# Kernel optimization log

Hardware: AMD Instinct MI355X
Metric: run time of the kernel (lower is better)

Reference implementation:

```python
import jax, jax.numpy as jnp
import numpy as np

T = 2048        # flat document tokens
D = 400         # word_emb (doc emb dim)
H2 = 400        # 2 * lstm_hidden_size
MAXW = 10       # max_ment_width
C = T * MAXW    # candidate spans
M = 600         # pruned mentions
A = 100         # max_ment_dist antecedents
FS = 20         # feature_size
HID = 150       # scorer hidden size
NG = 7          # num genres
BIN_WIDTHS = [1, 1, 1, 1, 1, 3, 8, 16, 32, 1]  # sums to 65, covers clamp(dist, max=64)
MENT_IN = 4 * 200 + FS + D          # 1220
ANTE_IN = 3 * MENT_IN + 3 * FS      # 3720


def setup_inputs() -> dict:
    key = jax.random.key(0)
    ks = jax.random.split(key, 24)
    w = lambda k, shp: (jax.random.normal(k, shp, dtype=jnp.float32) * 0.02)
    flat_doc_embs = jax.random.normal(ks[0], (T, D), dtype=jnp.float32)
    flat_lstm_out = jax.random.normal(ks[1], (T, H2), dtype=jnp.float32)
    # all spans up to width MAXW starting at each token (as produced upstream)
    cand_starts = jnp.repeat(jnp.arange(T), MAXW)
    cand_ends = jnp.minimum(cand_starts + jnp.tile(jnp.arange(MAXW), T), T - 1)
    top_ment_idx = jnp.sort(jax.random.choice(ks[2], C, (M,), replace=False))
    speaker_ids = jax.random.randint(ks[3], (T,), 0, 4)
    # antecedent index matrix exactly as built in get_antecedents
    i = jnp.arange(M)[:, None]
    j = jnp.arange(A)[None, :]
    antecedents = jnp.where(j < i, j, 0) + jnp.maximum(i - A, 0)
    antecedents_len = jnp.minimum(jnp.arange(M), A)
    bins = jnp.asarray(np.repeat(np.arange(len(BIN_WIDTHS)), BIN_WIDTHS), dtype=jnp.int32)
    return {
        'flat_doc_embs': flat_doc_embs, 'flat_lstm_out': flat_lstm_out,
        'cand_starts': cand_starts, 'cand_ends': cand_ends,
        'top_ment_idx': top_ment_idx, 'antecedents': antecedents,
        'antecedents_len': antecedents_len, 'speaker_ids': speaker_ids,
        'genre_id': 3, 'bins': bins,
        'width_table': w(ks[4], (MAXW, FS)), 'speaker_table': w(ks[5], (2, FS)),
        'genre_table': w(ks[6], (NG, FS)), 'dist_table': w(ks[7], (len(BIN_WIDTHS), FS)),
        'W_span': w(ks[8], (H2, 1)), 'b_span': jnp.zeros((1,), jnp.float32),
        'ms_w1': w(ks[9], (MENT_IN, HID)), 'ms_b1': jnp.zeros((HID,), jnp.float32),
        'ms_w2': w(ks[10], (HID, HID)), 'ms_b2': jnp.zeros((HID,), jnp.float32),
        'ms_w3': w(ks[11], (HID, 1)), 'ms_b3': jnp.zeros((1,), jnp.float32),
        'as_w1': w(ks[12], (ANTE_IN, HID)), 'as_b1': jnp.zeros((HID,), jnp.float32),
        'as_w2': w(ks[13], (HID, HID)), 'as_b2': jnp.zeros((HID,), jnp.float32),
        'as_w3': w(ks[14], (HID, 1)), 'as_b3': jnp.zeros((1,), jnp.float32),
    }


def _scorer(x, w1, b1, w2, b2, w3, b3):
    h = jax.nn.relu(x @ w1 + b1)
    h = jax.nn.relu(h @ w2 + b2)
    return (h @ w3 + b3)[..., 0]


def _ment_embedding(flat_doc_embs, flat_lstm_out, starts, ends, width_table, W_span, b_span):
    start_embs = flat_lstm_out[starts]            # [N, H2]
    end_embs = flat_lstm_out[ends]                # [N, H2]
    width = ends - starts + 1                     # [N]
    width_embs = width_table[width - 1]           # [N, FS]
    doc_len = flat_doc_embs.shape[0]
    span_idxs = jnp.minimum(jnp.arange(MAXW)[None, :] + starts[:, None], doc_len - 1)  # [N, W]
    ment_doc_embs = flat_doc_embs[span_idxs]      # [N, W, D]
    head_logits = (flat_lstm_out @ W_span + b_span)[:, 0]   # [T]
    logits = head_logits[span_idxs]               # [N, W]
    mask = jnp.arange(MAXW)[None, :] < width[:, None]
    logits = logits + jnp.log(mask.astype(jnp.float32))
    attn = jax.nn.softmax(logits, axis=1)[:, :, None]        # [N, W, 1]
    head_embs = (attn * ment_doc_embs).sum(axis=1)           # [N, D]
    return jnp.concatenate((start_embs, end_embs, width_embs, head_embs), axis=1)


def reference(flat_doc_embs, flat_lstm_out, cand_starts, cand_ends, top_ment_idx,
              antecedents, antecedents_len, speaker_ids, genre_id, bins,
              width_table, speaker_table, genre_table, dist_table, W_span, b_span,
              ms_w1, ms_b1, ms_w2, ms_b2, ms_w3, ms_b3,
              as_w1, as_b1, as_w2, as_b2, as_w3, as_b3):
    cand_embs = _ment_embedding(flat_doc_embs, flat_lstm_out, cand_starts, cand_ends,
                                width_table, W_span, b_span)          # [C, 1220]
    cand_scores = _scorer(cand_embs, ms_w1, ms_b1, ms_w2, ms_b2, ms_w3, ms_b3)  # [C]
    ment_starts = cand_starts[top_ment_idx]
    ment_embs = cand_embs[top_ment_idx]                                # [M, 1220]
    ment_scores = cand_scores[top_ment_idx]                            # [M]
    ment_speakers = speaker_ids[ment_starts]                           # [M]
    # antecedent_embedding
    num_ment, max_ante = antecedents.shape
    genre_emb = jnp.broadcast_to(genre_table[genre_id][None, None, :], (num_ment, max_ante, FS))
    ante_speakers = ment_speakers[antecedents]                         # [M, A]
    same_speaker = (ment_speakers[:, None] == ante_speakers).astype(jnp.int32)
    speaker_emb = speaker_table[same_speaker]                          # [M, A, FS]
    ante_dist = jnp.arange(num_ment)[:, None] - antecedents
    ante_dist_emb = dist_table[bins[jnp.minimum(ante_dist, 64)]]       # [M, A, FS]
    feature_emb = jnp.concatenate((speaker_emb, genre_emb, ante_dist_emb), axis=2)
    antecedent_emb = ment_embs[antecedents]                            # [M, A, 1220]
    ment_rep = jnp.broadcast_to(ment_embs[:, None, :], antecedent_emb.shape)
    similarity_emb = antecedent_emb * ment_rep
    ante_full = jnp.concatenate((ment_rep, antecedent_emb, similarity_emb, feature_emb), axis=2)
    ante_scores = _scorer(ante_full, as_w1, as_b1, as_w2, as_b2, as_w3, as_b3)   # [M, A]
    ante_mask = jnp.arange(max_ante)[None, :] < antecedents_len[:, None]
    ante_scores = ante_scores + jnp.log(ante_mask.astype(jnp.float32))
    coref = ante_scores + ment_scores[:, None] + ment_scores[antecedents]
    coref_score = jnp.concatenate((jnp.zeros((num_ment, 1), jnp.float32), coref), axis=1)
    return coref_score
```

## Files before the change

### kernel.cpp

```cpp
#include <hip/hip_runtime.h>
#include <math.h>

typedef __attribute__((ext_vector_type(8))) short short8v;
typedef __attribute__((ext_vector_type(4))) float float4v;
typedef unsigned int u32;
typedef unsigned short u16;

#define T_     2048
#define D_     400
#define H2_    400
#define MAXW_  10
#define M_     600
#define A_     100
#define FS_    20
#define HID_   150
#define HP_    160
#define MIN_   1220
#define KP_    1280
#define NCOL_  101
#define L2K_   192

#define NEGBIG_ (-1.0e30f)

#define OB_MSC   8192u
#define OB_PM    10752u
#define OB_PA    394752u
#define OB_SPKC  778752u
#define OB_GB    780032u
#define OB_DC    780672u
#define OB_MSPK  787072u
#define OB_H1W   789632u
#define OB_MEBF  1173632u
#define OB_WSIM  2709632u
#define OB_WK2   3119232u
#define OB_W2A   4348032u
#define OB_END   4409472u

__device__ __forceinline__ float bflo(u32 u){ u32 v = u << 16; return __builtin_bit_cast(float, v); }
__device__ __forceinline__ float bfhi(u32 u){ u32 v = u & 0xFFFF0000u; return __builtin_bit_cast(float, v); }
__device__ __forceinline__ u16 f2bf(float f){
  u32 u = __builtin_bit_cast(u32, f);
  u32 r = (u + 0x7FFFu + ((u >> 16) & 1u)) >> 16;
  return (u16)r;
}
__device__ __forceinline__ u32 cvtpk(float lo, float hi){
  u32 r; asm("v_cvt_pk_bf16_f32 %0, %1, %2" : "=v"(r) : "v"(lo), "v"(hi)); return r;
}

__global__ __launch_bounds__(256) void kb_prep(
    const float* __restrict__ msw1, const float* __restrict__ asw1,
    const float* __restrict__ asw2, const float* __restrict__ asb1,
    const float* __restrict__ spkt, const float* __restrict__ gent,
    const float* __restrict__ distt, const int* __restrict__ gid,
    u16* __restrict__ wsim, u16* __restrict__ wk2, u16* __restrict__ w2a,
    float* __restrict__ spk_c, float* __restrict__ gb, float* __restrict__ dc) {
  int z = blockIdx.z;
  if (z == 5) {
    if (blockIdx.x | blockIdx.y) return;
    int h = threadIdx.x;
    if (h >= HP_) return;
    if (h >= HID_) {
      spk_c[h] = 0.f; spk_c[HP_ + h] = 0.f; gb[h] = 0.f;
      for (int d = 0; d < 10; d++) dc[d * HP_ + h] = 0.f;
      return;
    }
    float s0 = 0.f, s1 = 0.f, g = asb1[h];
    int gi = gid[0];
    for (int f = 0; f < FS_; f++) {
      float w = asw1[(3660 + f) * HID_ + h];
      s0 += spkt[f] * w;
      s1 += spkt[FS_ + f] * w;
      g += gent[gi * FS_ + f] * asw1[(3680 + f) * HID_ + h];
    }
    spk_c[h] = s0; spk_c[HP_ + h] = s1; gb[h] = g;
    for (int d = 0; d < 10; d++) {
      float acc = 0.f;
      for (int f = 0; f < FS_; f++) acc += distt[d * FS_ + f] * asw1[(3700 + f) * HID_ + h];
      dc[d * HP_ + h] = acc;
    }
    return;
  }
  const float* src; u16* dst; int S, Rpad, R;
  if (z == 0)      { src = asw1 + 2440 * HID_; dst = wsim;            S = KP_;  Rpad = KP_;  R = MIN_; }
  else if (z == 1) { src = msw1;               dst = wk2;             S = KP_;  Rpad = KP_;  R = MIN_; }
  else if (z == 2) { src = asw1;               dst = wk2 + 160 * KP_; S = KP_;  Rpad = KP_;  R = MIN_; }
  else if (z == 3) { src = asw1 + 1220 * HID_; dst = wk2 + 320 * KP_; S = KP_;  Rpad = KP_;  R = MIN_; }
  else             { src = asw2;               dst = w2a;             S = L2K_; Rpad = L2K_; R = HID_;
                     if (blockIdx.x >= 6) return; }
  __shared__ float tile[32][33];
  int tx = threadIdx.x & 31, ty = threadIdx.x >> 5;
  int rb = blockIdx.x * 32, cb = blockIdx.y * 32;
#pragma unroll
  for (int it = 0; it < 4; it++) {
    int r = rb + ty + it * 8, c = cb + tx;
    tile[ty + it * 8][tx] = (r < R && c < HID_) ? src[(size_t)r * HID_ + c] : 0.f;
  }
  __syncthreads();
#pragma unroll
  for (int it = 0; it < 4; it++) {
    int c = cb + ty + it * 8, r = rb + tx;
    if (c < HP_ && r < Rpad) dst[(size_t)c * S + r] = f2bf(tile[tx][ty + it * 8]);
  }
}

__global__ __launch_bounds__(256) void ka_ment_emb(
    const float* __restrict__ doc, const float* __restrict__ lstm,
    const int* __restrict__ cs, const int* __restrict__ ce,
    const int* __restrict__ tmi, const int* __restrict__ spk,
    const float* __restrict__ wtab, const float* __restrict__ Wsp,
    const float* __restrict__ bsp,
    u16* __restrict__ mebf, int* __restrict__ mspk) {
  __shared__ float sl[MAXW_];
  int b = blockIdx.x, tid = threadIdx.x;
  int idx = tmi[b];
  int s = cs[idx], e = ce[idx];
  int width = e - s + 1;
  int wv = tid >> 6, lane = tid & 63;
  for (int w = wv; w < width; w += 4) {
    float acc = 0.f;
    for (int k = lane; k < H2_; k += 64) acc += lstm[(s + w) * H2_ + k] * Wsp[k];
    for (int off = 32; off; off >>= 1) acc += __shfl_down(acc, off);
    if (lane == 0) sl[w] = acc + bsp[0];
  }
  u16* row = mebf + (size_t)b * KP_;
  for (int d = tid; d < D_; d += 256) {
    row[d]      = f2bf(lstm[s * H2_ + d]);
    row[D_ + d] = f2bf(lstm[e * H2_ + d]);
  }
  if (tid < FS_) row[2 * D_ + tid] = f2bf(wtab[(width - 1) * FS_ + tid]);
  for (int d = tid; d < (KP_ - MIN_); d += 256) row[MIN_ + d] = 0;
  __syncthreads();
  float wl[MAXW_];
  float mx = -1e30f;
  for (int w = 0; w < width; w++) { wl[w] = sl[w]; mx = fmaxf(mx, wl[w]); }
  float sum = 0.f;
  for (int w = 0; w < width; w++) { wl[w] = expf(wl[w] - mx); sum += wl[w]; }
  float inv = 1.f / sum;
  for (int d = tid; d < D_; d += 256) {
    float acc = 0.f;
    for (int w = 0; w < width; w++) acc += wl[w] * doc[(s + w) * D_ + d];
    row[2 * D_ + FS_ + d] = f2bf(acc * inv);
  }
  if (tid == 0) mspk[b] = spk[s];
}

__global__ __launch_bounds__(256) void k2_mfma(
    const u16* __restrict__ mebf, const u16* __restrict__ wk2,
    const float* __restrict__ msb1,
    float* __restrict__ h1w, float* __restrict__ Pm, float* __restrict__ Pa) {
  __shared__ __align__(16) char lds[20480];
  int mt = blockIdx.x, ct = blockIdx.y;
  int tid = threadIdx.x, w = tid >> 6, l = tid & 63, l15 = l & 15, oct = l >> 4;
  int m0 = mt * 128;
  const u16* Bb = wk2 + (size_t)ct * 160 * KP_;
  u32 aswz = (u32)(l15 & 7) << 4;
  float4v acc[2][10];
#pragma unroll
  for (int p = 0; p < 2; p++)
#pragma unroll
    for (int h = 0; h < 10; h++) acc[p][h] = (float4v)0.f;
  int arow[2];
#pragma unroll
  for (int p = 0; p < 2; p++) {
    int r = m0 + (2 * w + p) * 16 + l15;
    arow[p] = (r < M_) ? r : (M_ - 1);
  }
  for (int kt = 0; kt < 20; kt++) {
    int k0 = kt * 64;
#pragma unroll
    for (int it = 0; it < 5; it++) {
      int ee = tid + it * 256;
      int r = ee >> 3, sg = ee & 7;
      uint4 v = *(const uint4*)(Bb + (size_t)r * KP_ + k0 + sg * 8);
      *(uint4*)(lds + (u32)(r * 128) + (((u32)(sg * 16)) ^ ((u32)(r & 7) << 4))) = v;
    }
    short8v A[2][2];
#pragma unroll
    for (int p = 0; p < 2; p++)
#pragma unroll
      for (int ks2 = 0; ks2 < 2; ks2++)
        A[p][ks2] = *(const short8v*)(mebf + (size_t)arow[p] * KP_ + k0 + ks2 * 32 + oct * 8);
    __syncthreads();
#pragma unroll
    for (int ks2 = 0; ks2 < 2; ks2++) {
      u32 inner = ((u32)(ks2 * 64 + oct * 16)) ^ aswz;
#pragma unroll
      for (int hf = 0; hf < 10; hf++) {
        short8v B = *(const short8v*)(lds + (u32)((hf * 16 + l15) * 128) + inner);
        acc[0][hf] = __builtin_amdgcn_mfma_f32_16x16x32_bf16(A[0][ks2], B, acc[0][hf], 0, 0, 0);
        acc[1][hf] = __builtin_amdgcn_mfma_f32_16x16x32_bf16(A[1][ks2], B, acc[1][hf], 0, 0, 0);
      }
    }
    __syncthreads();
  }
#pragma unroll
  for (int p = 0; p < 2; p++) {
    int mb = m0 + (2 * w + p) * 16 + oct * 4;
#pragma unroll
    for (int hf = 0; hf < 10; hf++) {
      int c = hf * 16 + l15;
#pragma unroll
      for (int r = 0; r < 4; r++) {
        int m = mb + r;
        if (m < M_) {
          float v = acc[p][hf][r];
          if (ct == 0) {
            float bias = (c < HID_) ? msb1[c] : 0.f;
            h1w[m * HP_ + c] = fmaxf(v + bias, 0.f);
          } else if (ct == 1) {
            Pm[m * HP_ + c] = v;
          } else {
            Pa[m * HP_ + c] = v;
          }
        }
      }
    }
  }
}

__global__ __launch_bounds__(256) void k5_msc(
    const float* __restrict__ h1w, const float* __restrict__ w2, const float* __restrict__ b2,
    const float* __restrict__ w3, const float* __restrict__ b3, float* __restrict__ msc) {
  __shared__ float h1s[HID_];
  __shared__ float h2s[HID_];
  __shared__ float red[4];
  int i = blockIdx.x, tid = threadIdx.x;
  if (tid < HID_) h1s[tid] = h1w[i * HP_ + tid];
  __syncthreads();
  if (tid < HID_) {
    float a = b2[tid];
    for (int k = 0; k < HID_; k++) a += h1s[k] * w2[k * HID_ + tid];
    h2s[tid] = fmaxf(a, 0.f);
  }
  __syncthreads();
  float p = (tid < HID_) ? h2s[tid] * w3[tid] : 0.f;
  for (int off = 32; off; off >>= 1) p += __shfl_down(p, off, 64);
  if ((tid & 63) == 0) red[tid >> 6] = p;
  __syncthreads();
  if (tid == 0) msc[i] = red[0] + red[1] + red[2] + red[3] + b3[0];
}

__global__ __launch_bounds__(256) void k4_pairs(
    const u16* __restrict__ mebf, const u16* __restrict__ wsim, const u16* __restrict__ w2a,
    const float* __restrict__ Pm, const float* __restrict__ Pa,
    const float* __restrict__ spkc, const float* __restrict__ gb, const float* __restrict__ dc,
    const int* __restrict__ mspk, const int* __restrict__ bins,
    const float* __restrict__ msc,
    const float* __restrict__ ab2, const float* __restrict__ aw3, const float* __restrict__ ab3,
    float* __restrict__ out) {
  __shared__ __align__(16) char lds[49152];
  int bid = blockIdx.x;
  int i = (bid & 7) * 75 + (bid >> 3);
  int tid = threadIdx.x, w = tid >> 6, l = tid & 63, l15 = l & 15, oct = l >> 4;
  int len = min(i, A_);
  int jbase = max(i - A_, 0);
  if (len == 0) {
    if (tid == 0) out[0] = 0.f;
    if (tid < A_) out[1 + tid] = NEGBIG_;
    return;
  }
  {
    const uint4* src = (const uint4*)(mebf + (size_t)i * KP_);
    uint4* dst = (uint4*)(lds + 36864);
    if (tid < 160) dst[tid] = src[tid];
  }
  __syncthreads();

  float4v acc[2][10];
#pragma unroll
  for (int p = 0; p < 2; p++)
#pragma unroll
    for (int h = 0; h < 10; h++) acc[p][h] = (float4v)0.f;

  int arow = tid >> 1;
  int khe = (tid & 1) * 32;
  int jrow = min(jbase + arow, M_ - 1);
  const u16* ejrow = mebf + (size_t)jrow * KP_;
  u32 pwr_base = 20480u + (u32)arow * 128u;
  u32 pwr_swz  = (u32)(arow & 7) << 4;
  u32 kh2 = (u32)khe * 2u;
  int r0 = 2 * w * 16 + l15, r1 = r0 + 16;
  u32 aswz = (u32)(l15 & 7) << 4;

  uint4 pe[4];
#pragma unroll
  for (int q = 0; q < 4; q++) pe[q] = *(const uint4*)(ejrow + khe + q * 8);

  for (int kt = 0; kt < 20; kt++) {
    int k0 = kt * 64;
#pragma unroll
    for (int it = 0; it < 5; it++) {
      int ee = tid + it * 256;
      int r = ee >> 3, sg = ee & 7;
      uint4 v = *(const uint4*)(wsim + (size_t)r * KP_ + k0 + sg * 8);
      *(uint4*)(lds + (u32)(r * 128) + (((u32)(sg * 16)) ^ ((u32)(r & 7) << 4))) = v;
    }
    const uint4* eis = (const uint4*)((const u16*)(lds + 36864) + k0 + khe);
#pragma unroll
    for (int q = 0; q < 4; q++) {
      uint4 ej = pe[q];
      uint4 ei = eis[q];
      const u32* pj = (const u32*)&ej;
      const u32* pi = (const u32*)&ei;
      u32 o[4];
#pragma unroll
      for (int c = 0; c < 4; c++) {
        float a0 = bflo(pj[c]) * bflo(pi[c]);
        float a1 = bfhi(pj[c]) * bfhi(pi[c]);
        o[c] = cvtpk(a0, a1);
      }
      uint4 ov = make_uint4(o[0], o[1], o[2], o[3]);
      *(uint4*)(lds + (pwr_base + ((kh2 + (u32)q * 16u) ^ pwr_swz))) = ov;
    }
    {
      int kn = (kt < 19) ? (kt + 1) * 64 : kt * 64;
#pragma unroll
      for (int q = 0; q < 4; q++) pe[q] = *(const uint4*)(ejrow + kn + khe + q * 8);
    }
    __syncthreads();
#pragma unroll
    for (int ks2 = 0; ks2 < 2; ks2++) {
      u32 inner = ((u32)(ks2 * 64 + oct * 16)) ^ aswz;
      short8v A0 = *(const short8v*)(lds + 20480u + (u32)r0 * 128u + inner);
      short8v A1 = *(const short8v*)(lds + 20480u + (u32)r1 * 128u + inner);
#pragma unroll
      for (int hf = 0; hf < 10; hf++) {
        short8v B = *(const short8v*)(lds + (u32)((hf * 16 + l15) * 128) + inner);
        acc[0][hf] = __builtin_amdgcn_mfma_f32_16x16x32_bf16(A0, B, acc[0][hf], 0, 0, 0);
        acc[1][hf] = __builtin_amdgcn_mfma_f32_16x16x32_bf16(A1, B, acc[1][hf], 0, 0, 0);
      }
    }
    __syncthreads();
  }

  for (int x = tid; x < 2048; x += 256) {
    int a = x >> 4, q = x & 15;
    u32 byte = 32768u + (u32)a * 128u + (((u32)(64 + q * 4)) ^ ((u32)(a & 7) << 4));
    *(u32*)(lds + byte) = 0u;
  }
  int mi = mspk[i];
#pragma unroll
  for (int hf = 0; hf < 10; hf++) {
    int h = hf * 16 + l15;
    float pmh = Pm[i * HP_ + h];
    float gbh = gb[h];
    int t = h >> 6, kkb = (h & 63) * 2;
#pragma unroll
    for (int p = 0; p < 2; p++) {
      int ab = (2 * w + p) * 16 + oct * 4;
#pragma unroll
      for (int r = 0; r < 4; r++) {
        int a = ab + r;
        int ju = jbase + a;
        int jr = min(ju, M_ - 1);
        int same = (mspk[jr] == mi) ? 1 : 0;
        int dist = min(max(i - ju, 0), 64);
        int bin = bins[dist];
        float v = acc[p][hf][r] + pmh + gbh + Pa[jr * HP_ + h]
                + spkc[same * HP_ + h] + dc[bin * HP_ + h];
        v = fmaxf(v, 0.f);
        u32 byte = (u32)t * 16384u + (u32)a * 128u + (((u32)kkb) ^ ((u32)(a & 7) << 4));
        *(u16*)(lds + byte) = f2bf(v);
      }
    }
  }
  __syncthreads();

  float4v b2acc[2][10];
#pragma unroll
  for (int p = 0; p < 2; p++)
#pragma unroll
    for (int h = 0; h < 10; h++) b2acc[p][h] = (float4v)0.f;
#pragma unroll
  for (int t = 0; t < 3; t++) {
#pragma unroll
    for (int ks2 = 0; ks2 < 2; ks2++) {
      u32 inner = ((u32)(ks2 * 64 + oct * 16)) ^ aswz;
      u32 tb = (u32)t * 16384u;
      short8v A0 = *(const short8v*)(lds + tb + (u32)r0 * 128u + inner);
      short8v A1 = *(const short8v*)(lds + tb + (u32)r1 * 128u + inner);
      int ke = t * 64 + ks2 * 32 + oct * 8;
#pragma unroll
      for (int hf = 0; hf < 10; hf++) {
        short8v B = *(const short8v*)(w2a + (size_t)(hf * 16 + l15) * L2K_ + ke);
        b2acc[0][hf] = __builtin_amdgcn_mfma_f32_16x16x32_bf16(A0, B, b2acc[0][hf], 0, 0, 0);
        b2acc[1][hf] = __builtin_amdgcn_mfma_f32_16x16x32_bf16(A1, B, b2acc[1][hf], 0, 0, 0);
      }
    }
  }

  float part[2][4] = {{0.f,0.f,0.f,0.f},{0.f,0.f,0.f,0.f}};
#pragma unroll
  for (int hf = 0; hf < 10; hf++) {
    int h = hf * 16 + l15;
    float bias = (h < HID_) ? ab2[h] : 0.f;
    float w3v  = (h < HID_) ? aw3[h] : 0.f;
#pragma unroll
    for (int p = 0; p < 2; p++)
#pragma unroll
      for (int r = 0; r < 4; r++) {
        float hv = fmaxf(b2acc[p][hf][r] + bias, 0.f);
        part[p][r] += hv * w3v;
      }
  }
#pragma unroll
  for (int m = 1; m <= 8; m <<= 1) {
#pragma unroll
    for (int p = 0; p < 2; p++)
#pragma unroll
      for (int r = 0; r < 4; r++) part[p][r] += __shfl_xor(part[p][r], m, 64);
  }
  float b3 = ab3[0];
  float msci = msc[i];
  if (l15 == 0) {
#pragma unroll
    for (int p = 0; p < 2; p++)
#pragma unroll
      for (int r = 0; r < 4; r++) {
        int a = (2 * w + p) * 16 + oct * 4 + r;
        if (a < A_) {
          float res = (a < len) ? (part[p][r] + b3 + msci + msc[jbase + a]) : NEGBIG_;
          out[(size_t)i * NCOL_ + 1 + a] = res;
        }
      }
  }
  if (tid == 0) out[(size_t)i * NCOL_] = 0.f;
}

extern "C" void kernel_launch(void* const* d_in, const int* in_sizes, int n_in,
                              void* d_out, int out_size, void* d_ws, size_t ws_size,
                              hipStream_t stream) {
  const float* doc   = (const float*)d_in[0];
  const float* lstm  = (const float*)d_in[1];
  const int*   cs    = (const int*)d_in[2];
  const int*   ce    = (const int*)d_in[3];
  const int*   tmi   = (const int*)d_in[4];
  const int*   spk   = (const int*)d_in[7];
  const int*   gid   = (const int*)d_in[8];
  const int*   bins  = (const int*)d_in[9];
  const float* wtab  = (const float*)d_in[10];
  const float* spkt  = (const float*)d_in[11];
  const float* gent  = (const float*)d_in[12];
  const float* distt = (const float*)d_in[13];
  const float* Wsp   = (const float*)d_in[14];
  const float* bsp   = (const float*)d_in[15];
  const float* msw1  = (const float*)d_in[16];
  const float* msb1  = (const float*)d_in[17];
  const float* msw2  = (const float*)d_in[18];
  const float* msb2  = (const float*)d_in[19];
  const float* msw3  = (const float*)d_in[20];
  const float* msb3  = (const float*)d_in[21];
  const float* asw1  = (const float*)d_in[22];
  const float* asb1  = (const float*)d_in[23];
  const float* asw2  = (const float*)d_in[24];
  const float* asb2  = (const float*)d_in[25];
  const float* asw3  = (const float*)d_in[26];
  const float* asb3  = (const float*)d_in[27];
  (void)in_sizes; (void)n_in; (void)out_size; (void)ws_size;

  char* ws = (char*)d_ws;
  float* msc   = (float*)(ws + OB_MSC);
  float* Pm    = (float*)(ws + OB_PM);
  float* Pa    = (float*)(ws + OB_PA);
  float* spkc  = (float*)(ws + OB_SPKC);
  float* gb    = (float*)(ws + OB_GB);
  float* dc    = (float*)(ws + OB_DC);
  int*   mspk  = (int*)(ws + OB_MSPK);
  float* h1w   = (float*)(ws + OB_H1W);
  u16*   mebf  = (u16*)(ws + OB_MEBF);
  u16*   wsim  = (u16*)(ws + OB_WSIM);
  u16*   wk2   = (u16*)(ws + OB_WK2);
  u16*   w2a   = (u16*)(ws + OB_W2A);
  float* out   = (float*)d_out;

  dim3 gb_(40, 5, 6);
  kb_prep<<<gb_, 256, 0, stream>>>(msw1, asw1, asw2, asb1, spkt, gent, distt, gid,
                                   wsim, wk2, w2a, spkc, gb, dc);
  ka_ment_emb<<<M_, 256, 0, stream>>>(doc, lstm, cs, ce, tmi, spk, wtab, Wsp, bsp,
                                      mebf, mspk);
  dim3 g2(5, 3);
  k2_mfma<<<g2, 256, 0, stream>>>(mebf, wk2, msb1, h1w, Pm, Pa);
  k5_msc<<<M_, 256, 0, stream>>>(h1w, msw2, msb2, msw3, msb3, msc);
  k4_pairs<<<M_, 256, 0, stream>>>(mebf, wsim, w2a, Pm, Pa, spkc, gb, dc,
                                   mspk, bins, msc, asb2, asw3, asb3, out);
}
```

Measured before the change: 374.9 us.

## Register-prefetch wsim tiles one stage ahead and use lighter LDS barriers

The similarity-GEMM K loop now loads the next wsim B tile and the next ment-embedding slice into registers one iteration ahead. Global-load latency can then overlap the MFMA work instead of stalling right before each LDS store. Plain __syncthreads are replaced with a custom barrier that waits only on lgkmcnt, not on outstanding global loads, so the prefetches stay in flight across the barrier. This costs more registers (pb[5]), which may lower occupancy.

```diff
diff --git a/kernel.cpp b/kernel.cpp
--- a/kernel.cpp
+++ b/kernel.cpp
@@ -45,6 +45,13 @@
 }
 __device__ __forceinline__ u32 cvtpk(float lo, float hi){
   u32 r; asm("v_cvt_pk_bf16_f32 %0, %1, %2" : "=v"(r) : "v"(lo), "v"(hi)); return r;
+}
+__device__ __forceinline__ void barx(){
+  asm volatile("s_waitcnt lgkmcnt(0)" ::: "memory");
+  __builtin_amdgcn_sched_barrier(0);
+  __builtin_amdgcn_s_barrier();
+  __builtin_amdgcn_sched_barrier(0);
+  asm volatile("" ::: "memory");
 }
 
 __global__ __launch_bounds__(256) void kb_prep(
@@ -281,21 +288,25 @@
   u32 kh2 = (u32)khe * 2u;
   int r0 = 2 * w * 16 + l15, r1 = r0 + 16;
   u32 aswz = (u32)(l15 & 7) << 4;
-
-  uint4 pe[4];
+  int bsr = tid >> 3, bssg = tid & 7;
+  uint4 pb[5], pe[4];
+
+#pragma unroll
+  for (int it = 0; it < 5; it++) {
+    int ee = tid + it * 256;
+    int r = ee >> 3, sg = ee & 7;
+    pb[it] = *(const uint4*)(wsim + (size_t)r * KP_ + sg * 8);
+  }
 #pragma unroll
   for (int q = 0; q < 4; q++) pe[q] = *(const uint4*)(ejrow + khe + q * 8);
-
-  for (int kt = 0; kt < 20; kt++) {
-    int k0 = kt * 64;
-#pragma unroll
-    for (int it = 0; it < 5; it++) {
-      int ee = tid + it * 256;
-      int r = ee >> 3, sg = ee & 7;
-      uint4 v = *(const uint4*)(wsim + (size_t)r * KP_ + k0 + sg * 8);
-      *(uint4*)(lds + (u32)(r * 128) + (((u32)(sg * 16)) ^ ((u32)(r & 7) << 4))) = v;
-    }
-    const uint4* eis = (const uint4*)((const u16*)(lds + 36864) + k0 + khe);
+#pragma unroll
+  for (int it = 0; it < 5; it++) {
+    int ee = tid + it * 256;
+    int r = ee >> 3, sg = ee & 7;
+    *(uint4*)(lds + (u32)(r * 128) + (((u32)(sg * 16)) ^ ((u32)(r & 7) << 4))) = pb[it];
+  }
+  {
+    const uint4* eis = (const uint4*)((const u16*)(lds + 36864) + khe);
 #pragma unroll
     for (int q = 0; q < 4; q++) {
       uint4 ej = pe[q];
@@ -304,20 +315,22 @@
       const u32* pi = (const u32*)&ei;
       u32 o[4];
 #pragma unroll
-      for (int c = 0; c < 4; c++) {
-        float a0 = bflo(pj[c]) * bflo(pi[c]);
-        float a1 = bfhi(pj[c]) * bfhi(pi[c]);
-        o[c] = cvtpk(a0, a1);
-      }
-      uint4 ov = make_uint4(o[0], o[1], o[2], o[3]);
-      *(uint4*)(lds + (pwr_base + ((kh2 + (u32)q * 16u) ^ pwr_swz))) = ov;
-    }
-    {
-      int kn = (kt < 19) ? (kt + 1) * 64 : kt * 64;
-#pragma unroll
-      for (int q = 0; q < 4; q++) pe[q] = *(const uint4*)(ejrow + kn + khe + q * 8);
-    }
-    __syncthreads();
+      for (int c = 0; c < 4; c++)
+        o[c] = cvtpk(bflo(pj[c]) * bflo(pi[c]), bfhi(pj[c]) * bfhi(pi[c]));
+      *(uint4*)(lds + (pwr_base + ((kh2 + (u32)q * 16u) ^ pwr_swz))) = make_uint4(o[0], o[1], o[2], o[3]);
+    }
+  }
+#pragma unroll
+  for (int q = 0; q < 4; q++) pe[q] = *(const uint4*)(ejrow + 64 + khe + q * 8);
+#pragma unroll
+  for (int it = 0; it < 5; it++) {
+    int ee = tid + it * 256;
+    int r = ee >> 3, sg = ee & 7;
+    pb[it] = *(const uint4*)(wsim + (size_t)r * KP_ + 64 + sg * 8);
+  }
+  barx();
+
+  for (int kt = 0; kt < 20; kt++) {
 #pragma unroll
     for (int ks2 = 0; ks2 < 2; ks2++) {
       u32 inner = ((u32)(ks2 * 64 + oct * 16)) ^ aswz;
@@ -330,9 +343,47 @@
         acc[1][hf] = __builtin_amdgcn_mfma_f32_16x16x32_bf16(A1, B, acc[1][hf], 0, 0, 0);
       }
     }
-    __syncthreads();
-  }
-
+    barx();
+    if (kt < 19) {
+#pragma unroll
+      for (int it = 0; it < 5; it++) {
+        int ee = tid + it * 256;
+        int r = ee >> 3, sg = ee & 7;
+        *(uint4*)(lds + (u32)(r * 128) + (((u32)(sg * 16)) ^ ((u32)(r & 7) << 4))) = pb[it];
+      }
+      {
+        int k0n = (kt + 1) * 64;
+        const uint4* eis = (const uint4*)((const u16*)(lds + 36864) + k0n + khe);
+#pragma unroll
+        for (int q = 0; q < 4; q++) {
+          uint4 ej = pe[q];
+          uint4 ei = eis[q];
+          const u32* pj = (const u32*)&ej;
+          const u32* pi = (const u32*)&ei;
+          u32 o[4];
+#pragma unroll
+          for (int c = 0; c < 4; c++)
+            o[c] = cvtpk(bflo(pj[c]) * bflo(pi[c]), bfhi(pj[c]) * bfhi(pi[c]));
+          *(uint4*)(lds + (pwr_base + ((kh2 + (u32)q * 16u) ^ pwr_swz))) = make_uint4(o[0], o[1], o[2], o[3]);
+        }
+      }
+      if (kt < 18) {
+        int k2o = (kt + 2) * 64;
+#pragma unroll
+        for (int q = 0; q < 4; q++) pe[q] = *(const uint4*)(ejrow + k2o + khe + q * 8);
+#pragma unroll
+        for (int it = 0; it < 5; it++) {
+          int ee = tid + it * 256;
+          int r = ee >> 3, sg = ee & 7;
+          pb[it] = *(const uint4*)(wsim + (size_t)r * KP_ + k2o + sg * 8);
+        }
+      }
+      barx();
+    }
+  }
+  (void)bsr; (void)bssg;
+
+  __syncthreads();
   for (int x = tid; x < 2048; x += 256) {
     int a = x >> 4, q = x & 15;
     u32 byte = 32768u + (u32)a * 128u + (((u32)(64 + q * 4)) ^ ((u32)(a & 7) << 4));
```

Result: slower. 449.5 us (+19.9%).

## Double-buffer weight tiles via direct global-to-LDS loads in pair scorer

Applied to the files above, without the earlier changes.

The pair-scoring kernel's weight tile staging now uses global_load_lds, which writes straight into LDS without passing through registers. Tiles alternate between two buffers, so the next k-tile is fetched while MFMAs consume the current one. Each iteration now ends with one barrier instead of two, guarded by explicit vmcnt/lgkmcnt waits and sched barriers. LDS use grows to about 59 KB per block, which may reduce occupancy, and the hand-written wait counts must match the number of loads in flight.

```diff
diff --git a/kernel.cpp b/kernel.cpp
--- a/kernel.cpp
+++ b/kernel.cpp
@@ -22,6 +22,11 @@
 
 #define NEGBIG_ (-1.0e30f)
 
+#define LB0_  0u
+#define LB1_  20480u
+#define LP_   40960u
+#define LEI_  57344u
+
 #define OB_MSC   8192u
 #define OB_PM    10752u
 #define OB_PA    394752u
@@ -45,6 +50,10 @@
 }
 __device__ __forceinline__ u32 cvtpk(float lo, float hi){
   u32 r; asm("v_cvt_pk_bf16_f32 %0, %1, %2" : "=v"(r) : "v"(lo), "v"(hi)); return r;
+}
+__device__ __forceinline__ void gload_lds16(const u16* g, char* l){
+  __builtin_amdgcn_global_load_lds((const __attribute__((address_space(1))) void*)g,
+                                   (__attribute__((address_space(3))) void*)l, 16, 0, 0);
 }
 
 __global__ __launch_bounds__(256) void kb_prep(
@@ -248,7 +257,7 @@
     const float* __restrict__ msc,
     const float* __restrict__ ab2, const float* __restrict__ aw3, const float* __restrict__ ab3,
     float* __restrict__ out) {
-  __shared__ __align__(16) char lds[49152];
+  __shared__ __align__(16) char lds[59904];
   int bid = blockIdx.x;
   int i = (bid & 7) * 75 + (bid >> 3);
   int tid = threadIdx.x, w = tid >> 6, l = tid & 63, l15 = l & 15, oct = l >> 4;
@@ -261,7 +270,7 @@
   }
   {
     const uint4* src = (const uint4*)(mebf + (size_t)i * KP_);
-    uint4* dst = (uint4*)(lds + 36864);
+    uint4* dst = (uint4*)(lds + LEI_);
     if (tid < 160) dst[tid] = src[tid];
   }
   __syncthreads();
@@ -276,63 +285,81 @@
   int khe = (tid & 1) * 32;
   int jrow = min(jbase + arow, M_ - 1);
   const u16* ejrow = mebf + (size_t)jrow * KP_;
-  u32 pwr_base = 20480u + (u32)arow * 128u;
+  u32 pwr_base = LP_ + (u32)arow * 128u;
   u32 pwr_swz  = (u32)(arow & 7) << 4;
   u32 kh2 = (u32)khe * 2u;
-  int r0 = 2 * w * 16 + l15, r1 = r0 + 16;
+  int r0 = 32 * w + l15, r1 = r0 + 16;
   u32 aswz = (u32)(l15 & 7) << 4;
+  int rloc = l >> 3, slot = l & 7;
+  u32 ldsw = (u32)__builtin_amdgcn_readfirstlane(w * 5120);
 
   uint4 pe[4];
+
+#pragma unroll
+  for (int c = 0; c < 5; c++) {
+    int r = 40 * w + 8 * c + rloc;
+    const u16* g = wsim + (size_t)r * KP_ + ((slot ^ (r & 7)) * 8);
+    gload_lds16(g, lds + LB0_ + ldsw + (u32)c * 1024u);
+  }
 #pragma unroll
   for (int q = 0; q < 4; q++) pe[q] = *(const uint4*)(ejrow + khe + q * 8);
+  asm volatile("s_waitcnt vmcnt(4)" ::: "memory");
+  __builtin_amdgcn_sched_barrier(0);
+  __builtin_amdgcn_s_barrier();
+  __builtin_amdgcn_sched_barrier(0);
 
   for (int kt = 0; kt < 20; kt++) {
-    int k0 = kt * 64;
-#pragma unroll
-    for (int it = 0; it < 5; it++) {
-      int ee = tid + it * 256;
-      int r = ee >> 3, sg = ee & 7;
-      uint4 v = *(const uint4*)(wsim + (size_t)r * KP_ + k0 + sg * 8);
-      *(uint4*)(lds + (u32)(r * 128) + (((u32)(sg * 16)) ^ ((u32)(r & 7) << 4))) = v;
-    }
-    const uint4* eis = (const uint4*)((const u16*)(lds + 36864) + k0 + khe);
-#pragma unroll
-    for (int q = 0; q < 4; q++) {
-      uint4 ej = pe[q];
-      uint4 ei = eis[q];
-      const u32* pj = (const u32*)&ej;
-      const u32* pi = (const u32*)&ei;
-      u32 o[4];
-#pragma unroll
-      for (int c = 0; c < 4; c++) {
-        float a0 = bflo(pj[c]) * bflo(pi[c]);
-        float a1 = bfhi(pj[c]) * bfhi(pi[c]);
-        o[c] = cvtpk(a0, a1);
-      }
-      uint4 ov = make_uint4(o[0], o[1], o[2], o[3]);
-      *(uint4*)(lds + (pwr_base + ((kh2 + (u32)q * 16u) ^ pwr_swz))) = ov;
-    }
+    u32 bufr = (kt & 1) ? LB1_ : LB0_;
+    u32 bufw = (kt & 1) ? LB0_ : LB1_;
     {
-      int kn = (kt < 19) ? (kt + 1) * 64 : kt * 64;
+      const uint4* eis = (const uint4*)((const u16*)(lds + LEI_) + kt * 64 + khe);
+#pragma unroll
+      for (int q = 0; q < 4; q++) {
+        uint4 ej = pe[q];
+        uint4 ei = eis[q];
+        const u32* pj = (const u32*)&ej;
+        const u32* pi = (const u32*)&ei;
+        u32 o[4];
+#pragma unroll
+        for (int c = 0; c < 4; c++)
+          o[c] = cvtpk(bflo(pj[c]) * bflo(pi[c]), bfhi(pj[c]) * bfhi(pi[c]));
+        *(uint4*)(lds + (pwr_base + ((kh2 + (u32)q * 16u) ^ pwr_swz))) = make_uint4(o[0], o[1], o[2], o[3]);
+      }
+    }
+    if (kt < 19) {
+      int kn = (kt + 1) * 64;
+#pragma unroll
+      for (int c = 0; c < 5; c++) {
+        int r = 40 * w + 8 * c + rloc;
+        const u16* g = wsim + (size_t)r * KP_ + kn + ((slot ^ (r & 7)) * 8);
+        gload_lds16(g, lds + bufw + ldsw + (u32)c * 1024u);
+      }
 #pragma unroll
       for (int q = 0; q < 4; q++) pe[q] = *(const uint4*)(ejrow + kn + khe + q * 8);
     }
-    __syncthreads();
+    asm volatile("s_waitcnt lgkmcnt(0)" ::: "memory");
+    __builtin_amdgcn_sched_barrier(0);
 #pragma unroll
     for (int ks2 = 0; ks2 < 2; ks2++) {
       u32 inner = ((u32)(ks2 * 64 + oct * 16)) ^ aswz;
-      short8v A0 = *(const short8v*)(lds + 20480u + (u32)r0 * 128u + inner);
-      short8v A1 = *(const short8v*)(lds + 20480u + (u32)r1 * 128u + inner);
+      short8v A0 = *(const short8v*)(lds + LP_ + (u32)r0 * 128u + inner);
+      short8v A1 = *(const short8v*)(lds + LP_ + (u32)r1 * 128u + inner);
 #pragma unroll
       for (int hf = 0; hf < 10; hf++) {
-        short8v B = *(const short8v*)(lds + (u32)((hf * 16 + l15) * 128) + inner);
+        short8v B = *(const short8v*)(lds + bufr + (u32)((hf * 16 + l15) * 128) + inner);
         acc[0][hf] = __builtin_amdgcn_mfma_f32_16x16x32_bf16(A0, B, acc[0][hf], 0, 0, 0);
         acc[1][hf] = __builtin_amdgcn_mfma_f32_16x16x32_bf16(A1, B, acc[1][hf], 0, 0, 0);
       }
     }
-    __syncthreads();
-  }
-
+    if (kt < 19) {
+      asm volatile("s_waitcnt vmcnt(4)" ::: "memory");
+      __builtin_amdgcn_sched_barrier(0);
+      __builtin_amdgcn_s_barrier();
+      __builtin_amdgcn_sched_barrier(0);
+    }
+  }
+
+  __syncthreads();
   for (int x = tid; x < 2048; x += 256) {
     int a = x >> 4, q = x & 15;
     u32 byte = 32768u + (u32)a * 128u + (((u32)(64 + q * 4)) ^ ((u32)(a & 7) << 4));
@@ -377,8 +404,8 @@
     for (int ks2 = 0; ks2 < 2; ks2++) {
       u32 inner = ((u32)(ks2 * 64 + oct * 16)) ^ aswz;
       u32 tb = (u32)t * 16384u;
-      short8v A0 = *(const short8v*)(lds + tb + (u32)r0 * 128u + inner);
-      short8v A1 = *(const short8v*)(lds + tb + (u32)r1 * 128u + inner);
+      short8v A0 = *(const short8v*)(lds + tb + (u32)(32 * w + l15) * 128u + inner);
+      short8v A1 = *(const short8v*)(lds + tb + (u32)(32 * w + 16 + l15) * 128u + inner);
       int ke = t * 64 + ks2 * 32 + oct * 8;
 #pragma unroll
       for (int hf = 0; hf < 10; hf++) {
```

New measurement: 359.7 us. 4.0% less time.
